# Kernel tuning notes

Hardware: AMD Instinct MI355X
Metric: run time of the kernel (lower is better)

Reference implementation:

```python
import math
import jax, jax.numpy as jnp
import numpy as np

D_MODEL = 1024
N_HEADS = 16
D_K = D_MODEL // N_HEADS
LQ, LK, B = 2048, 2048, 2


def setup_inputs() -> dict:
    key = jax.random.key(0)
    ks = jax.random.split(key, 12)
    q = jax.random.normal(ks[0], (LQ, B, D_MODEL), dtype=jnp.float32)
    k = jax.random.normal(ks[1], (LK, B, D_MODEL), dtype=jnp.float32)
    v = jax.random.normal(ks[2], (LK, B, D_MODEL), dtype=jnp.float32)
    # causal mask: scores with mask==0 are filled with -1e9
    mask = jnp.tril(jnp.ones((LQ, LK), dtype=jnp.int32))
    s = 0.02
    w_q = jax.random.normal(ks[3], (D_MODEL, D_MODEL), jnp.float32) * s
    b_q = jnp.zeros((D_MODEL,), jnp.float32)
    w_k = jax.random.normal(ks[4], (D_MODEL, D_MODEL), jnp.float32) * s
    b_k = jnp.zeros((D_MODEL,), jnp.float32)
    w_v = jax.random.normal(ks[5], (D_MODEL, D_MODEL), jnp.float32) * s
    b_v = jnp.zeros((D_MODEL,), jnp.float32)
    w_o = jax.random.normal(ks[6], (D_MODEL, D_MODEL), jnp.float32) * s
    b_o = jnp.zeros((D_MODEL,), jnp.float32)
    return {"query": q, "key": k, "value": v, "mask": mask,
            "w_q": w_q, "b_q": b_q, "w_k": w_k, "b_k": b_k,
            "w_v": w_v, "b_v": b_v, "w_o": w_o, "b_o": b_o}


def reference(query, key, value, mask, w_q, b_q, w_k, b_k, w_v, b_v, w_o, b_o):
    # dropout layers are identity (eval mode)
    Lq, Bsz, D = query.shape
    Lk = key.shape[0]
    scale = math.sqrt(D_K)
    # seq-first linear projections, then [L,B,D] -> [B,H,L,dk]
    def proj(x, w, b, L):
        y = x @ w.T + b
        return y.reshape(L, Bsz, N_HEADS, D_K).transpose(1, 2, 0, 3)
    Q = proj(query, w_q, b_q, Lq)   # [B,H,Lq,dk]
    K = proj(key, w_k, b_k, Lk)     # [B,H,Lk,dk]
    V = proj(value, w_v, b_v, Lk)   # [B,H,Lk,dk]
    scores = jnp.einsum('bhqd,bhkd->bhqk', Q, K) / scale
    m = mask[None, None, :, :]  # 2D mask broadcast path of original
    scores = jnp.where(m == 0, jnp.float32(-1e9), scores)
    attn = jax.nn.softmax(scores, axis=-1)  # [B,H,Lq,Lk]
    out = jnp.einsum('bhqk,bhkd->bhqd', attn, V)  # [B,H,Lq,dk]
    # replicate torch: transpose(0,1) -> [H,B,Lq,dk], flat view to [Lq,B,D]
    out = jnp.transpose(out, (1, 0, 2, 3)).reshape(Lq, Bsz, D)
    output = out @ w_o.T + b_o
    return output, attn
```

## Files before the change

### kernel.cpp

```cpp
#include <hip/hip_runtime.h>
#include <cstdint>

#define DM    1024
#define NH    16
#define DKH   64
#define SEQ   2048
#define BSZ   2
#define MROWS 4096
#define QB    128
#define K2    128

typedef __attribute__((ext_vector_type(8))) short bf16x8;
typedef __attribute__((ext_vector_type(4))) float f32x4;

__device__ __forceinline__ f32x4 mfma16(bf16x8 a, bf16x8 b, f32x4 c){
  return __builtin_amdgcn_mfma_f32_16x16x32_bf16(a, b, c, 0, 0, 0);
}

__device__ __forceinline__ ushort f2bf(float f){
  unsigned u = __float_as_uint(f);
  return (ushort)((u + 0x7FFFu + ((u >> 16) & 1u)) >> 16);
}

__device__ __forceinline__ void gload16(const ushort* g, ushort* l){
  __builtin_amdgcn_global_load_lds(
      (const __attribute__((address_space(1))) void*)g,
      (__attribute__((address_space(3))) void*)l, 16, 0, 0);
}

__device__ __forceinline__ void ntstore4(float* p, f32x4 v){
  __builtin_nontemporal_store(v, (f32x4*)p);
}

__global__ void cast_all(const float* __restrict__ q, const float* __restrict__ k,
                         const float* __restrict__ v, const float* __restrict__ wq,
                         const float* __restrict__ wk, const float* __restrict__ wv,
                         const float* __restrict__ wo,
                         ushort* __restrict__ qb, ushort* __restrict__ kb,
                         ushort* __restrict__ vb, ushort* __restrict__ wqb,
                         ushort* __restrict__ wkb, ushort* __restrict__ wvb,
                         ushort* __restrict__ wob)
{
  const int NB = (MROWS*DM)/4;
  const int NW = (DM*DM)/4;
  int stride = gridDim.x*blockDim.x;
  for (int i = blockIdx.x*blockDim.x + threadIdx.x; i < 3*NB; i += stride){
    int sel = i >> 20, j = i & (NB-1);
    const float4 x = ((const float4*)(sel==0?q:sel==1?k:v))[j];
    ushort4 o; o.x=f2bf(x.x); o.y=f2bf(x.y); o.z=f2bf(x.z); o.w=f2bf(x.w);
    ((ushort4*)(sel==0?qb:sel==1?kb:vb))[j] = o;
  }
  for (int i = blockIdx.x*blockDim.x + threadIdx.x; i < 4*NW; i += stride){
    int sel = i >> 18, j = i & (NW-1);
    const float4 x = ((const float4*)(sel==0?wq:sel==1?wk:sel==2?wv:wo))[j];
    ushort4 o; o.x=f2bf(x.x); o.y=f2bf(x.y); o.z=f2bf(x.z); o.w=f2bf(x.w);
    ((ushort4*)(sel==0?wqb:sel==1?wkb:sel==2?wvb:wob))[j] = o;
  }
}

template<int OUT_F32>
__device__ __forceinline__ void gemm_body(const ushort* __restrict__ A,
                                          const ushort* __restrict__ W,
                                          const float* __restrict__ bias,
                                          void* __restrict__ outp)
{
  __shared__ ushort As[128*32];
  __shared__ ushort Bs[128*32];
  const int tid = threadIdx.x, w = tid>>6, l = tid&63;
  const int wr = w>>1, wc = w&1, lr = l&15, lg = l>>4;
  const int bm = blockIdx.x, bn = blockIdx.y;
  const ushort* Ab = A + (size_t)bm*128*DM;
  const ushort* Wb = W + (size_t)bn*128*DM;
  f32x4 z4 = {0.f,0.f,0.f,0.f};
  f32x4 acc[4][4];
  #pragma unroll
  for (int i=0;i<4;i++){ acc[i][0]=z4; acc[i][1]=z4; acc[i][2]=z4; acc[i][3]=z4; }

  for (int k0 = 0; k0 < DM; k0 += 32){
    __syncthreads();
    #pragma unroll
    for (int i=0;i<2;i++){
      int idx = w*2+i;
      int row = idx*16 + (l>>2);
      int cg  = (l&3)*8;
      gload16(&Ab[(size_t)row*DM + k0 + cg], &As[idx*512]);
      gload16(&Wb[(size_t)row*DM + k0 + cg], &Bs[idx*512]);
    }
    __syncthreads();
    bf16x8 af[4], bw[4];
    #pragma unroll
    for (int t=0;t<4;t++) af[t] = *(const bf16x8*)&As[(wr*64 + t*16 + lr)*32 + lg*8];
    #pragma unroll
    for (int t=0;t<4;t++) bw[t] = *(const bf16x8*)&Bs[(wc*64 + t*16 + lr)*32 + lg*8];
    #pragma unroll
    for (int tm=0;tm<4;tm++)
      #pragma unroll
      for (int tn=0;tn<4;tn++)
        acc[tm][tn] = mfma16(af[tm], bw[tn], acc[tm][tn]);
  }
  #pragma unroll
  for (int tn=0;tn<4;tn++){
    int col = bn*128 + wc*64 + tn*16 + lr;
    float bv = bias[col];
    #pragma unroll
    for (int tm=0;tm<4;tm++){
      #pragma unroll
      for (int r=0;r<4;r++){
        int row = bm*128 + wr*64 + tm*16 + lg*4 + r;
        float val = acc[tm][tn][r] + bv;
        if (OUT_F32) ((float*)outp)[(size_t)row*DM + col] = val;
        else ((ushort*)outp)[(size_t)row*DM + col] = f2bf(val);
      }
    }
  }
}

__global__ __launch_bounds__(256) void gemm_qkv(
    const ushort* __restrict__ A0, const ushort* __restrict__ A1, const ushort* __restrict__ A2,
    const ushort* __restrict__ W0, const ushort* __restrict__ W1, const ushort* __restrict__ W2,
    const float* __restrict__ b0, const float* __restrict__ b1, const float* __restrict__ b2,
    ushort* __restrict__ O0, ushort* __restrict__ O1, ushort* __restrict__ O2)
{
  int z = blockIdx.z;
  const ushort* A = (z==0)?A0:((z==1)?A1:A2);
  const ushort* W = (z==0)?W0:((z==1)?W1:W2);
  const float*  b = (z==0)?b0:((z==1)?b1:b2);
  ushort*       O = (z==0)?O0:((z==1)?O1:O2);
  gemm_body<0>(A, W, b, O);
}

__global__ __launch_bounds__(256) void gemm_fin(const ushort* __restrict__ A,
                                                const ushort* __restrict__ W,
                                                const float* __restrict__ b,
                                                float* __restrict__ O)
{
  gemm_body<1>(A, W, b, O);
}

__global__ __launch_bounds__(256) void transpose_v(const ushort* __restrict__ Vp,
                                                   ushort* __restrict__ Vt)
{
  __shared__ ushort Ts[64*72];
  const int lt = blockIdx.x;
  const int h  = blockIdx.y;
  const int b  = blockIdx.z;
  const int tid = threadIdx.x;
  const int sr = tid>>3, sc = (tid&7)*8;
  uint4 v0 = *(const uint4*)&Vp[((size_t)(lt*64+sr)*BSZ + b)*DM + h*DKH + sc];
  uint4 v1 = *(const uint4*)&Vp[((size_t)(lt*64+sr+32)*BSZ + b)*DM + h*DKH + sc];
  const ushort* p0 = (const ushort*)&v0;
  const ushort* p1 = (const ushort*)&v1;
  #pragma unroll
  for (int j=0;j<8;j++){
    Ts[(sc+j)*72 + sr]    = p0[j];
    Ts[(sc+j)*72 + sr+32] = p1[j];
  }
  __syncthreads();
  const size_t ob = (size_t)((b*NH+h)*DKH);
  *(uint4*)&Vt[(ob + sr)*SEQ + lt*64 + sc]    = *(const uint4*)&Ts[sr*72 + sc];
  *(uint4*)&Vt[(ob + sr+32)*SEQ + lt*64 + sc] = *(const uint4*)&Ts[(sr+32)*72 + sc];
}

__global__ __launch_bounds__(512, 4) void attn_fused(const ushort* __restrict__ Qp,
                                                     const ushort* __restrict__ Kp,
                                                     const ushort* __restrict__ Vt,
                                                     float* __restrict__ attn,
                                                     ushort* __restrict__ ctx)
{
  __shared__ ushort Ks[K2*72];
  __shared__ ushort Vs[64*136];
  __shared__ ushort Ps[8][16*72];
  const int bid0 = blockIdx.x;
  const int xcd = bid0 & 7, slot = bid0 >> 3;
  const int grp = xcd + 8*(slot>>4);
  const int qb  = 15 - (slot & 15);
  const int h = grp & 15, b = grp >> 4;
  const int tid = threadIdx.x, w = tid>>6, l = tid&63;
  const int lr = l&15, lg = l>>4;
  const int q0 = qb*QB;
  const int rounds = qb + 1;
  ushort* Pw = &Ps[w][0];
  const size_t attnBase = (size_t)(b*NH+h)*SEQ*SEQ;
  const size_t vtBase   = (size_t)((b*NH+h)*DKH);
  const int qrow = q0 + w*16;
  const int wmax = qrow + 15;

  const int sKr = tid>>3,  sKc = (tid&7)*8;
  const int sVr = tid>>4,  sVc = (tid&15)*8;
  const ushort* Kg = Kp + (size_t)b*DM + h*DKH;
  const ushort* Vg = Vt + vtBase*SEQ;

  bf16x8 aq0 = *(const bf16x8*)&Qp[((size_t)(qrow+lr)*BSZ + b)*DM + h*DKH + lg*8];
  bf16x8 aq1 = *(const bf16x8*)&Qp[((size_t)(qrow+lr)*BSZ + b)*DM + h*DKH + 32 + lg*8];

  float rs[4] = {0.f,0.f,0.f,0.f};
  uint4 ka0 = *(const uint4*)&Kg[(size_t)(sKr)*BSZ*DM + sKc];
  uint4 ka1 = *(const uint4*)&Kg[(size_t)(sKr+64)*BSZ*DM + sKc];
  for (int r = 0; r < rounds; r++){
    __syncthreads();
    *(uint4*)&Ks[sKr*72+sKc]      = ka0;
    *(uint4*)&Ks[(sKr+64)*72+sKc] = ka1;
    if (r+1 < rounds){
      ka0 = *(const uint4*)&Kg[(size_t)((r+1)*K2+sKr)*BSZ*DM + sKc];
      ka1 = *(const uint4*)&Kg[(size_t)((r+1)*K2+sKr+64)*BSZ*DM + sKc];
    }
    __syncthreads();
    #pragma unroll
    for (int hh=0; hh<2; hh++){
      int kbase = r*K2 + hh*64;
      if (kbase > wmax) break;
      #pragma unroll
      for (int nt=0; nt<4; nt++){
        f32x4 s4 = {0.f,0.f,0.f,0.f};
        bf16x8 bk0 = *(const bf16x8*)&Ks[(hh*64+nt*16+lr)*72 + lg*8];
        bf16x8 bk1 = *(const bf16x8*)&Ks[(hh*64+nt*16+lr)*72 + 32 + lg*8];
        s4 = mfma16(aq0, bk0, s4);
        s4 = mfma16(aq1, bk1, s4);
        int kc = kbase + nt*16 + lr;
        #pragma unroll
        for (int r4=0;r4<4;r4++){
          int qr = qrow + lg*4 + r4;
          float e = exp2f(s4[r4]*0.18033688011112042f);
          rs[r4] += (kc <= qr) ? e : 0.f;
        }
      }
    }
  }
  float rinv[4];
  #pragma unroll
  for (int r4=0;r4<4;r4++){
    float vs = rs[r4];
    vs += __shfl_xor(vs, 1, 16);
    vs += __shfl_xor(vs, 2, 16);
    vs += __shfl_xor(vs, 4, 16);
    vs += __shfl_xor(vs, 8, 16);
    rinv[r4] = 1.0f / vs;
  }

  f32x4 z4 = {0.f,0.f,0.f,0.f};
  f32x4 oacc[4] = {z4,z4,z4,z4};
  uint4 kb0 = *(const uint4*)&Kg[(size_t)(sKr)*BSZ*DM + sKc];
  uint4 kb1 = *(const uint4*)&Kg[(size_t)(sKr+64)*BSZ*DM + sKc];
  uint4 vb0 = *(const uint4*)&Vg[(size_t)(sVr)*SEQ + sVc];
  uint4 vb1 = *(const uint4*)&Vg[(size_t)(sVr+32)*SEQ + sVc];
  for (int r = 0; r < rounds; r++){
    __syncthreads();
    *(uint4*)&Ks[sKr*72+sKc]        = kb0;
    *(uint4*)&Ks[(sKr+64)*72+sKc]   = kb1;
    *(uint4*)&Vs[sVr*136+sVc]       = vb0;
    *(uint4*)&Vs[(sVr+32)*136+sVc]  = vb1;
    if (r+1 < rounds){
      kb0 = *(const uint4*)&Kg[(size_t)((r+1)*K2+sKr)*BSZ*DM + sKc];
      kb1 = *(const uint4*)&Kg[(size_t)((r+1)*K2+sKr+64)*BSZ*DM + sKc];
      vb0 = *(const uint4*)&Vg[(size_t)(sVr)*SEQ + (r+1)*K2 + sVc];
      vb1 = *(const uint4*)&Vg[(size_t)(sVr+32)*SEQ + (r+1)*K2 + sVc];
    }
    __syncthreads();
    #pragma unroll
    for (int hh=0; hh<2; hh++){
      int kbase = r*K2 + hh*64;
      if (kbase <= wmax){
        #pragma unroll
        for (int nt=0; nt<4; nt++){
          f32x4 s4 = {0.f,0.f,0.f,0.f};
          bf16x8 bk0 = *(const bf16x8*)&Ks[(hh*64+nt*16+lr)*72 + lg*8];
          bf16x8 bk1 = *(const bf16x8*)&Ks[(hh*64+nt*16+lr)*72 + 32 + lg*8];
          s4 = mfma16(aq0, bk0, s4);
          s4 = mfma16(aq1, bk1, s4);
          int kc = kbase + nt*16 + lr;
          #pragma unroll
          for (int r4=0;r4<4;r4++){
            int qg = qrow + lg*4 + r4;
            float p = (kc <= qg) ? exp2f(s4[r4]*0.18033688011112042f)*rinv[r4] : 0.f;
            Pw[(lg*4+r4)*72 + nt*16 + lr] = f2bf(p);
          }
        }
        #pragma unroll
        for (int pass=0; pass<4; pass++){
          int row = pass*4 + lg;
          ushort4 pv = *(const ushort4*)&Pw[row*72 + lr*4];
          f32x4 o;
          o.x = __uint_as_float(((unsigned)pv.x) << 16);
          o.y = __uint_as_float(((unsigned)pv.y) << 16);
          o.z = __uint_as_float(((unsigned)pv.z) << 16);
          o.w = __uint_as_float(((unsigned)pv.w) << 16);
          ntstore4(&attn[attnBase + (size_t)(qrow + row)*SEQ + kbase + lr*4], o);
        }
        bf16x8 pa0 = *(const bf16x8*)&Pw[lr*72 + lg*8];
        bf16x8 pa1 = *(const bf16x8*)&Pw[lr*72 + 32 + lg*8];
        #pragma unroll
        for (int nt=0; nt<4; nt++){
          bf16x8 vv0 = *(const bf16x8*)&Vs[(nt*16+lr)*136 + hh*64 + lg*8];
          bf16x8 vv1 = *(const bf16x8*)&Vs[(nt*16+lr)*136 + hh*64 + 32 + lg*8];
          oacc[nt] = mfma16(pa0, vv0, oacc[nt]);
          oacc[nt] = mfma16(pa1, vv1, oacc[nt]);
        }
      } else {
        f32x4 zz = {0.f,0.f,0.f,0.f};
        #pragma unroll
        for (int pass=0; pass<4; pass++){
          int row = pass*4 + lg;
          ntstore4(&attn[attnBase + (size_t)(qrow + row)*SEQ + kbase + lr*4], zz);
        }
      }
    }
  }
  #pragma unroll
  for (int nt=0;nt<4;nt++){
    #pragma unroll
    for (int r4=0;r4<4;r4++){
      int qg = qrow + lg*4 + r4;
      ctx[((size_t)(h*BSZ+b)*SEQ + qg)*DKH + nt*16 + lr] = f2bf(oacc[nt][r4]);
    }
  }
  int z0 = rounds*K2;
  if (z0 < SEQ){
    f32x4 zz = {0.f,0.f,0.f,0.f};
    for (int r16=0; r16<16; r16++){
      float* rowp = attn + attnBase + (size_t)(qrow + r16)*SEQ;
      for (int c = z0 + l*4; c < SEQ; c += 256)
        ntstore4(&rowp[c], zz);
    }
  }
}

extern "C" void kernel_launch(void* const* d_in, const int* in_sizes, int n_in,
                              void* d_out, int out_size, void* d_ws, size_t ws_size,
                              hipStream_t stream)
{
  (void)in_sizes; (void)n_in; (void)out_size; (void)ws_size;
  const float* q  = (const float*)d_in[0];
  const float* k  = (const float*)d_in[1];
  const float* v  = (const float*)d_in[2];
  const float* wq = (const float*)d_in[4];
  const float* bq = (const float*)d_in[5];
  const float* wk = (const float*)d_in[6];
  const float* bk = (const float*)d_in[7];
  const float* wv = (const float*)d_in[8];
  const float* bv = (const float*)d_in[9];
  const float* wo = (const float*)d_in[10];
  const float* bo = (const float*)d_in[11];

  char* ws = (char*)d_ws;
  const size_t SZ_BIG = (size_t)MROWS*DM*2;
  const size_t SZ_W   = (size_t)DM*DM*2;
  ushort* Qb  = (ushort*)(ws);
  ushort* Kb  = (ushort*)(ws + SZ_BIG);
  ushort* Vb  = (ushort*)(ws + 2*SZ_BIG);
  ushort* Wqb = (ushort*)(ws + 3*SZ_BIG);
  ushort* Wkb = (ushort*)(ws + 3*SZ_BIG + SZ_W);
  ushort* Wvb = (ushort*)(ws + 3*SZ_BIG + 2*SZ_W);
  ushort* Wob = (ushort*)(ws + 3*SZ_BIG + 3*SZ_W);
  ushort* Qp  = (ushort*)(ws + 3*SZ_BIG + 4*SZ_W);
  ushort* Kp  = (ushort*)(ws + 4*SZ_BIG + 4*SZ_W);
  ushort* Vp  = (ushort*)(ws + 5*SZ_BIG + 4*SZ_W);
  ushort* Ctx = (ushort*)(ws + 6*SZ_BIG + 4*SZ_W);
  ushort* Vt  = Qb;

  float* out  = (float*)d_out;
  float* attn = out + (size_t)SEQ*BSZ*DM;

  cast_all<<<2048, 256, 0, stream>>>(q,k,v,wq,wk,wv,wo, Qb,Kb,Vb,Wqb,Wkb,Wvb,Wob);
  dim3 gq(32, 8, 3);
  gemm_qkv<<<gq, 256, 0, stream>>>(Qb,Kb,Vb, Wqb,Wkb,Wvb, bq,bk,bv, Qp,Kp,Vp);
  dim3 gt(32, NH, BSZ);
  transpose_v<<<gt, 256, 0, stream>>>(Vp, Vt);
  attn_fused<<<512, 512, 0, stream>>>(Qp, Kp, Vt, attn, Ctx);
  dim3 gf(32, 8, 1);
  gemm_fin<<<gf, 256, 0, stream>>>(Ctx, Wob, bo, out);
}
```

Before: 239.0 us.

## Shrink attention query tile to 64 with balanced causal scheduling; smaller output GEMM tiles

The attention kernel moves from 128-row query blocks with 512 threads to 64-row query blocks with 256 threads, using 64-key rounds. The grid doubles to 1024 blocks, and the query-tile order interleaves heavy and light causal tiles so work balances across CUs. This removes the half-masked 64-key sub-tiles and the branch that skipped them inside 128-key rounds. The output projection GEMM gets a separate 64x128-tile kernel that doubles its block count for better CU fill. In exchange, K and V tiles are reloaded more often per query row and there are more block-level barriers.

Result: faster. 217.1 us (-9.2%).

```diff
diff --git a/kernel.cpp b/kernel.cpp
--- a/kernel.cpp
+++ b/kernel.cpp
@@ -7,8 +7,6 @@
 #define SEQ   2048
 #define BSZ   2
 #define MROWS 4096
-#define QB    128
-#define K2    128
 
 typedef __attribute__((ext_vector_type(8))) short bf16x8;
 typedef __attribute__((ext_vector_type(4))) float f32x4;
@@ -58,11 +56,10 @@
   }
 }
 
-template<int OUT_F32>
-__device__ __forceinline__ void gemm_body(const ushort* __restrict__ A,
-                                          const ushort* __restrict__ W,
-                                          const float* __restrict__ bias,
-                                          void* __restrict__ outp)
+__device__ __forceinline__ void gemm_body128(const ushort* __restrict__ A,
+                                             const ushort* __restrict__ W,
+                                             const float* __restrict__ bias,
+                                             ushort* __restrict__ outp)
 {
   __shared__ ushort As[128*32];
   __shared__ ushort Bs[128*32];
@@ -107,9 +104,7 @@
       #pragma unroll
       for (int r=0;r<4;r++){
         int row = bm*128 + wr*64 + tm*16 + lg*4 + r;
-        float val = acc[tm][tn][r] + bv;
-        if (OUT_F32) ((float*)outp)[(size_t)row*DM + col] = val;
-        else ((ushort*)outp)[(size_t)row*DM + col] = f2bf(val);
+        outp[(size_t)row*DM + col] = f2bf(acc[tm][tn][r] + bv);
       }
     }
   }
@@ -126,15 +121,65 @@
   const ushort* W = (z==0)?W0:((z==1)?W1:W2);
   const float*  b = (z==0)?b0:((z==1)?b1:b2);
   ushort*       O = (z==0)?O0:((z==1)?O1:O2);
-  gemm_body<0>(A, W, b, O);
-}
-
-__global__ __launch_bounds__(256) void gemm_fin(const ushort* __restrict__ A,
-                                                const ushort* __restrict__ W,
-                                                const float* __restrict__ b,
-                                                float* __restrict__ O)
-{
-  gemm_body<1>(A, W, b, O);
+  gemm_body128(A, W, b, O);
+}
+
+__global__ __launch_bounds__(256) void gemm_fin64(const ushort* __restrict__ A,
+                                                  const ushort* __restrict__ W,
+                                                  const float* __restrict__ bias,
+                                                  float* __restrict__ O)
+{
+  __shared__ ushort As[64*32];
+  __shared__ ushort Bs[128*32];
+  const int tid = threadIdx.x, w = tid>>6, l = tid&63;
+  const int wr = w>>1, wc = w&1, lr = l&15, lg = l>>4;
+  const int bm = blockIdx.x, bn = blockIdx.y;
+  const ushort* Ab = A + (size_t)bm*64*DM;
+  const ushort* Wb = W + (size_t)bn*128*DM;
+  f32x4 z4 = {0.f,0.f,0.f,0.f};
+  f32x4 acc[2][4];
+  #pragma unroll
+  for (int i=0;i<2;i++){ acc[i][0]=z4; acc[i][1]=z4; acc[i][2]=z4; acc[i][3]=z4; }
+
+  for (int k0 = 0; k0 < DM; k0 += 32){
+    __syncthreads();
+    {
+      int row = w*16 + (l>>2);
+      int cg  = (l&3)*8;
+      gload16(&Ab[(size_t)row*DM + k0 + cg], &As[w*512]);
+    }
+    #pragma unroll
+    for (int i=0;i<2;i++){
+      int idx = w*2+i;
+      int row = idx*16 + (l>>2);
+      int cg  = (l&3)*8;
+      gload16(&Wb[(size_t)row*DM + k0 + cg], &Bs[idx*512]);
+    }
+    __syncthreads();
+    bf16x8 af[2], bw[4];
+    #pragma unroll
+    for (int t=0;t<2;t++) af[t] = *(const bf16x8*)&As[(wr*32 + t*16 + lr)*32 + lg*8];
+    #pragma unroll
+    for (int t=0;t<4;t++) bw[t] = *(const bf16x8*)&Bs[(wc*64 + t*16 + lr)*32 + lg*8];
+    #pragma unroll
+    for (int tm=0;tm<2;tm++)
+      #pragma unroll
+      for (int tn=0;tn<4;tn++)
+        acc[tm][tn] = mfma16(af[tm], bw[tn], acc[tm][tn]);
+  }
+  #pragma unroll
+  for (int tn=0;tn<4;tn++){
+    int col = bn*128 + wc*64 + tn*16 + lr;
+    float bv = bias[col];
+    #pragma unroll
+    for (int tm=0;tm<2;tm++){
+      #pragma unroll
+      for (int r=0;r<4;r++){
+        int row = bm*64 + wr*32 + tm*16 + lg*4 + r;
+        O[(size_t)row*DM + col] = acc[tm][tn][r] + bv;
+      }
+    }
+  }
 }
 
 __global__ __launch_bounds__(256) void transpose_v(const ushort* __restrict__ Vp,
@@ -161,68 +206,60 @@
   *(uint4*)&Vt[(ob + sr+32)*SEQ + lt*64 + sc] = *(const uint4*)&Ts[(sr+32)*72 + sc];
 }
 
-__global__ __launch_bounds__(512, 4) void attn_fused(const ushort* __restrict__ Qp,
+__global__ __launch_bounds__(256, 5) void attn_fused(const ushort* __restrict__ Qp,
                                                      const ushort* __restrict__ Kp,
                                                      const ushort* __restrict__ Vt,
                                                      float* __restrict__ attn,
                                                      ushort* __restrict__ ctx)
 {
-  __shared__ ushort Ks[K2*72];
-  __shared__ ushort Vs[64*136];
-  __shared__ ushort Ps[8][16*72];
+  __shared__ ushort Ks[64*72];
+  __shared__ ushort Vs[64*72];
+  __shared__ ushort Ps[4][16*72];
   const int bid0 = blockIdx.x;
   const int xcd = bid0 & 7, slot = bid0 >> 3;
-  const int grp = xcd + 8*(slot>>4);
-  const int qb  = 15 - (slot & 15);
+  const int grp = xcd + 8*(slot & 3);
+  const int ds  = slot >> 2;
+  const int qt  = (ds & 1) ? (ds >> 1) : (31 - (ds >> 1));
   const int h = grp & 15, b = grp >> 4;
+  const int q0 = qt*64;
+  const int rounds = qt + 1;
   const int tid = threadIdx.x, w = tid>>6, l = tid&63;
   const int lr = l&15, lg = l>>4;
-  const int q0 = qb*QB;
-  const int rounds = qb + 1;
   ushort* Pw = &Ps[w][0];
   const size_t attnBase = (size_t)(b*NH+h)*SEQ*SEQ;
-  const size_t vtBase   = (size_t)((b*NH+h)*DKH);
   const int qrow = q0 + w*16;
-  const int wmax = qrow + 15;
-
-  const int sKr = tid>>3,  sKc = (tid&7)*8;
-  const int sVr = tid>>4,  sVc = (tid&15)*8;
+  const int sr = tid>>3, sc = (tid&7)*8;
   const ushort* Kg = Kp + (size_t)b*DM + h*DKH;
-  const ushort* Vg = Vt + vtBase*SEQ;
+  const ushort* Vg = Vt + (size_t)((b*NH+h)*DKH)*SEQ;
 
   bf16x8 aq0 = *(const bf16x8*)&Qp[((size_t)(qrow+lr)*BSZ + b)*DM + h*DKH + lg*8];
   bf16x8 aq1 = *(const bf16x8*)&Qp[((size_t)(qrow+lr)*BSZ + b)*DM + h*DKH + 32 + lg*8];
 
   float rs[4] = {0.f,0.f,0.f,0.f};
-  uint4 ka0 = *(const uint4*)&Kg[(size_t)(sKr)*BSZ*DM + sKc];
-  uint4 ka1 = *(const uint4*)&Kg[(size_t)(sKr+64)*BSZ*DM + sKc];
+  uint4 ka0 = *(const uint4*)&Kg[(size_t)(sr)*BSZ*DM + sc];
+  uint4 ka1 = *(const uint4*)&Kg[(size_t)(sr+32)*BSZ*DM + sc];
   for (int r = 0; r < rounds; r++){
     __syncthreads();
-    *(uint4*)&Ks[sKr*72+sKc]      = ka0;
-    *(uint4*)&Ks[(sKr+64)*72+sKc] = ka1;
+    *(uint4*)&Ks[sr*72+sc]      = ka0;
+    *(uint4*)&Ks[(sr+32)*72+sc] = ka1;
     if (r+1 < rounds){
-      ka0 = *(const uint4*)&Kg[(size_t)((r+1)*K2+sKr)*BSZ*DM + sKc];
-      ka1 = *(const uint4*)&Kg[(size_t)((r+1)*K2+sKr+64)*BSZ*DM + sKc];
-    }
-    __syncthreads();
-    #pragma unroll
-    for (int hh=0; hh<2; hh++){
-      int kbase = r*K2 + hh*64;
-      if (kbase > wmax) break;
-      #pragma unroll
-      for (int nt=0; nt<4; nt++){
-        f32x4 s4 = {0.f,0.f,0.f,0.f};
-        bf16x8 bk0 = *(const bf16x8*)&Ks[(hh*64+nt*16+lr)*72 + lg*8];
-        bf16x8 bk1 = *(const bf16x8*)&Ks[(hh*64+nt*16+lr)*72 + 32 + lg*8];
-        s4 = mfma16(aq0, bk0, s4);
-        s4 = mfma16(aq1, bk1, s4);
-        int kc = kbase + nt*16 + lr;
-        #pragma unroll
-        for (int r4=0;r4<4;r4++){
-          int qr = qrow + lg*4 + r4;
-          float e = exp2f(s4[r4]*0.18033688011112042f);
-          rs[r4] += (kc <= qr) ? e : 0.f;
-        }
+      ka0 = *(const uint4*)&Kg[(size_t)((r+1)*64+sr)*BSZ*DM + sc];
+      ka1 = *(const uint4*)&Kg[(size_t)((r+1)*64+sr+32)*BSZ*DM + sc];
+    }
+    __syncthreads();
+    #pragma unroll
+    for (int nt=0; nt<4; nt++){
+      f32x4 s4 = {0.f,0.f,0.f,0.f};
+      bf16x8 bk0 = *(const bf16x8*)&Ks[(nt*16+lr)*72 + lg*8];
+      bf16x8 bk1 = *(const bf16x8*)&Ks[(nt*16+lr)*72 + 32 + lg*8];
+      s4 = mfma16(aq0, bk0, s4);
+      s4 = mfma16(aq1, bk1, s4);
+      int kc = r*64 + nt*16 + lr;
+      #pragma unroll
+      for (int r4=0;r4<4;r4++){
+        int qr = qrow + lg*4 + r4;
+        float e = exp2f(s4[r4]*0.18033688011112042f);
+        rs[r4] += (kc <= qr) ? e : 0.f;
       }
     }
   }
@@ -239,70 +276,58 @@
 
   f32x4 z4 = {0.f,0.f,0.f,0.f};
   f32x4 oacc[4] = {z4,z4,z4,z4};
-  uint4 kb0 = *(const uint4*)&Kg[(size_t)(sKr)*BSZ*DM + sKc];
-  uint4 kb1 = *(const uint4*)&Kg[(size_t)(sKr+64)*BSZ*DM + sKc];
-  uint4 vb0 = *(const uint4*)&Vg[(size_t)(sVr)*SEQ + sVc];
-  uint4 vb1 = *(const uint4*)&Vg[(size_t)(sVr+32)*SEQ + sVc];
+  uint4 kb0 = *(const uint4*)&Kg[(size_t)(sr)*BSZ*DM + sc];
+  uint4 kb1 = *(const uint4*)&Kg[(size_t)(sr+32)*BSZ*DM + sc];
+  uint4 vb0 = *(const uint4*)&Vg[(size_t)(sr)*SEQ + sc];
+  uint4 vb1 = *(const uint4*)&Vg[(size_t)(sr+32)*SEQ + sc];
   for (int r = 0; r < rounds; r++){
     __syncthreads();
-    *(uint4*)&Ks[sKr*72+sKc]        = kb0;
-    *(uint4*)&Ks[(sKr+64)*72+sKc]   = kb1;
-    *(uint4*)&Vs[sVr*136+sVc]       = vb0;
-    *(uint4*)&Vs[(sVr+32)*136+sVc]  = vb1;
+    *(uint4*)&Ks[sr*72+sc]      = kb0;
+    *(uint4*)&Ks[(sr+32)*72+sc] = kb1;
+    *(uint4*)&Vs[sr*72+sc]      = vb0;
+    *(uint4*)&Vs[(sr+32)*72+sc] = vb1;
     if (r+1 < rounds){
-      kb0 = *(const uint4*)&Kg[(size_t)((r+1)*K2+sKr)*BSZ*DM + sKc];
-      kb1 = *(const uint4*)&Kg[(size_t)((r+1)*K2+sKr+64)*BSZ*DM + sKc];
-      vb0 = *(const uint4*)&Vg[(size_t)(sVr)*SEQ + (r+1)*K2 + sVc];
-      vb1 = *(const uint4*)&Vg[(size_t)(sVr+32)*SEQ + (r+1)*K2 + sVc];
-    }
-    __syncthreads();
-    #pragma unroll
-    for (int hh=0; hh<2; hh++){
-      int kbase = r*K2 + hh*64;
-      if (kbase <= wmax){
-        #pragma unroll
-        for (int nt=0; nt<4; nt++){
-          f32x4 s4 = {0.f,0.f,0.f,0.f};
-          bf16x8 bk0 = *(const bf16x8*)&Ks[(hh*64+nt*16+lr)*72 + lg*8];
-          bf16x8 bk1 = *(const bf16x8*)&Ks[(hh*64+nt*16+lr)*72 + 32 + lg*8];
-          s4 = mfma16(aq0, bk0, s4);
-          s4 = mfma16(aq1, bk1, s4);
-          int kc = kbase + nt*16 + lr;
-          #pragma unroll
-          for (int r4=0;r4<4;r4++){
-            int qg = qrow + lg*4 + r4;
-            float p = (kc <= qg) ? exp2f(s4[r4]*0.18033688011112042f)*rinv[r4] : 0.f;
-            Pw[(lg*4+r4)*72 + nt*16 + lr] = f2bf(p);
-          }
-        }
-        #pragma unroll
-        for (int pass=0; pass<4; pass++){
-          int row = pass*4 + lg;
-          ushort4 pv = *(const ushort4*)&Pw[row*72 + lr*4];
-          f32x4 o;
-          o.x = __uint_as_float(((unsigned)pv.x) << 16);
-          o.y = __uint_as_float(((unsigned)pv.y) << 16);
-          o.z = __uint_as_float(((unsigned)pv.z) << 16);
-          o.w = __uint_as_float(((unsigned)pv.w) << 16);
-          ntstore4(&attn[attnBase + (size_t)(qrow + row)*SEQ + kbase + lr*4], o);
-        }
-        bf16x8 pa0 = *(const bf16x8*)&Pw[lr*72 + lg*8];
-        bf16x8 pa1 = *(const bf16x8*)&Pw[lr*72 + 32 + lg*8];
-        #pragma unroll
-        for (int nt=0; nt<4; nt++){
-          bf16x8 vv0 = *(const bf16x8*)&Vs[(nt*16+lr)*136 + hh*64 + lg*8];
-          bf16x8 vv1 = *(const bf16x8*)&Vs[(nt*16+lr)*136 + hh*64 + 32 + lg*8];
-          oacc[nt] = mfma16(pa0, vv0, oacc[nt]);
-          oacc[nt] = mfma16(pa1, vv1, oacc[nt]);
-        }
-      } else {
-        f32x4 zz = {0.f,0.f,0.f,0.f};
-        #pragma unroll
-        for (int pass=0; pass<4; pass++){
-          int row = pass*4 + lg;
-          ntstore4(&attn[attnBase + (size_t)(qrow + row)*SEQ + kbase + lr*4], zz);
-        }
+      kb0 = *(const uint4*)&Kg[(size_t)((r+1)*64+sr)*BSZ*DM + sc];
+      kb1 = *(const uint4*)&Kg[(size_t)((r+1)*64+sr+32)*BSZ*DM + sc];
+      vb0 = *(const uint4*)&Vg[(size_t)(sr)*SEQ + (r+1)*64 + sc];
+      vb1 = *(const uint4*)&Vg[(size_t)(sr+32)*SEQ + (r+1)*64 + sc];
+    }
+    __syncthreads();
+    const int k0 = r*64;
+    #pragma unroll
+    for (int nt=0; nt<4; nt++){
+      f32x4 s4 = {0.f,0.f,0.f,0.f};
+      bf16x8 bk0 = *(const bf16x8*)&Ks[(nt*16+lr)*72 + lg*8];
+      bf16x8 bk1 = *(const bf16x8*)&Ks[(nt*16+lr)*72 + 32 + lg*8];
+      s4 = mfma16(aq0, bk0, s4);
+      s4 = mfma16(aq1, bk1, s4);
+      int kc = k0 + nt*16 + lr;
+      #pragma unroll
+      for (int r4=0;r4<4;r4++){
+        int qg = qrow + lg*4 + r4;
+        float p = (kc <= qg) ? exp2f(s4[r4]*0.18033688011112042f)*rinv[r4] : 0.f;
+        Pw[(lg*4+r4)*72 + nt*16 + lr] = f2bf(p);
       }
+    }
+    #pragma unroll
+    for (int pass=0; pass<4; pass++){
+      int row16 = pass*4 + lg;
+      ushort4 pv = *(const ushort4*)&Pw[row16*72 + lr*4];
+      f32x4 o;
+      o.x = __uint_as_float(((unsigned)pv.x) << 16);
+      o.y = __uint_as_float(((unsigned)pv.y) << 16);
+      o.z = __uint_as_float(((unsigned)pv.z) << 16);
+      o.w = __uint_as_float(((unsigned)pv.w) << 16);
+      ntstore4(&attn[attnBase + (size_t)(qrow + row16)*SEQ + k0 + lr*4], o);
+    }
+    bf16x8 pa0 = *(const bf16x8*)&Pw[lr*72 + lg*8];
+    bf16x8 pa1 = *(const bf16x8*)&Pw[lr*72 + 32 + lg*8];
+    #pragma unroll
+    for (int nt=0; nt<4; nt++){
+      bf16x8 vv0 = *(const bf16x8*)&Vs[(nt*16+lr)*72 + lg*8];
+      bf16x8 vv1 = *(const bf16x8*)&Vs[(nt*16+lr)*72 + 32 + lg*8];
+      oacc[nt] = mfma16(pa0, vv0, oacc[nt]);
+      oacc[nt] = mfma16(pa1, vv1, oacc[nt]);
     }
   }
   #pragma unroll
@@ -313,7 +338,7 @@
       ctx[((size_t)(h*BSZ+b)*SEQ + qg)*DKH + nt*16 + lr] = f2bf(oacc[nt][r4]);
     }
   }
-  int z0 = rounds*K2;
+  int z0 = rounds*64;
   if (z0 < SEQ){
     f32x4 zz = {0.f,0.f,0.f,0.f};
     for (int r16=0; r16<16; r16++){
@@ -365,7 +390,7 @@
   gemm_qkv<<<gq, 256, 0, stream>>>(Qb,Kb,Vb, Wqb,Wkb,Wvb, bq,bk,bv, Qp,Kp,Vp);
   dim3 gt(32, NH, BSZ);
   transpose_v<<<gt, 256, 0, stream>>>(Vp, Vt);
-  attn_fused<<<512, 512, 0, stream>>>(Qp, Kp, Vt, attn, Ctx);
-  dim3 gf(32, 8, 1);
-  gemm_fin<<<gf, 256, 0, stream>>>(Ctx, Wob, bo, out);
-}
+  attn_fused<<<1024, 256, 0, stream>>>(Qp, Kp, Vt, attn, Ctx);
+  dim3 gf(64, 8, 1);
+  gemm_fin64<<<gf, 256, 0, stream>>>(Ctx, Wob, bo, out);
+}
```
